# Optimization experiments

Measured on AMD Instinct MI355X. Metric: run time of the kernel, lower is better.

## Reference

```python
import jax, jax.numpy as jnp
import numpy as np

NUM_CLASSES = 19


def setup_inputs() -> dict:
    key = jax.random.key(0)
    k1, k2 = jax.random.split(key)
    B, H, W, G = 32, 1024, 1024, 32
    n_blocks = B * (H // G) * (W // G)  # 32768
    preds = jax.random.normal(k1, (n_blocks, NUM_CLASSES), dtype=jnp.float32)
    targets = jax.random.randint(k2, (B, H, W), 0, NUM_CLASSES, dtype=jnp.int32)
    return {"preds": preds, "targets": targets, "grid_size": G}


def _get_batch_label_vector(targets, num_classes, grid_size):
    # targets: [B,H,W] int labels. Pad with `num_classes` (a value outside the
    # histogram range [0, num_classes-1], matching torch.histc's exclusion).
    b, h, w = targets.shape
    pad_h = (-h) % grid_size
    pad_w = (-w) % grid_size
    t = jnp.pad(targets, ((0, 0), (0, pad_h), (0, pad_w)),
                constant_values=num_classes)
    H, W = h + pad_h, w + pad_w
    # -> [n_blocks, grid_size*grid_size] of per-cell labels
    t = t.reshape(b, H // grid_size, grid_size, W // grid_size, grid_size)
    t = t.transpose(0, 1, 3, 2, 4).reshape(-1, grid_size * grid_size)
    n = t.shape[0]
    # Multi-hot presence vector via scatter; padded value == num_classes is
    # out of range and dropped (mirrors histc ignoring out-of-range values).
    tvect = jnp.zeros((n, num_classes), jnp.float32)
    tvect = tvect.at[jnp.arange(n)[:, None], t].set(1.0, mode='drop')
    return tvect


def reference(preds, targets, grid_size):
    se_target = _get_batch_label_vector(targets, NUM_CLASSES, grid_size)
    # BCE(sigmoid(preds), se_target) with mean reduction, written stably:
    # log(sigmoid(x)) = log_sigmoid(x), log(1-sigmoid(x)) = log_sigmoid(-x)
    log_p = jax.nn.log_sigmoid(preds)
    log_1mp = jax.nn.log_sigmoid(-preds)
    loss = -(se_target * log_p + (1.0 - se_target) * log_1mp)
    return jnp.mean(loss)
```

## Files before the change

### kernel.cpp

```cpp
#include <hip/hip_runtime.h>

#define NUM_CLASSES 19
#define TILES_PER_WAVE 8
#define WAVES_PER_BLOCK 4

__global__ __launch_bounds__(256) void seg_loss_partial(
    const float* __restrict__ preds,
    const int*   __restrict__ targets,
    float*       __restrict__ partial)
{
    const int t    = threadIdx.x;
    const int wave = t >> 6;
    const int lane = t & 63;

    float loss = 0.0f;
    const int tile0 = (blockIdx.x * WAVES_PER_BLOCK + wave) * TILES_PER_WAVE;

    for (int i = 0; i < TILES_PER_WAVE; ++i) {
        const int n  = tile0 + i;
        const int b  = n >> 10;
        const int by = (n >> 5) & 31;
        const int bx = n & 31;
        const int* base = targets + ((long long)b << 20)
                                  + (long long)(by << 5) * 1024
                                  + (bx << 5);

        unsigned mask = 0u;
        #pragma unroll
        for (int j = 0; j < 4; ++j) {
            const int idx  = j * 64 + lane;
            const int row  = idx >> 3;
            const int quad = idx & 7;
            const int4 v = *(const int4*)(base + row * 1024 + quad * 4);
            mask |= (1u << v.x) | (1u << v.y) | (1u << v.z) | (1u << v.w);
        }

        mask |= __shfl_xor(mask, 1);
        mask |= __shfl_xor(mask, 2);
        mask |= __shfl_xor(mask, 4);
        mask |= __shfl_xor(mask, 8);
        mask |= __shfl_xor(mask, 16);
        mask |= __shfl_xor(mask, 32);

        if (lane < NUM_CLASSES) {
            const float x  = preds[n * NUM_CLASSES + lane];
            const float tv = ((mask >> lane) & 1u) ? 1.0f : 0.0f;
            const float sp = fmaxf(x, 0.0f) + log1pf(__expf(-fabsf(x)));
            loss += sp - tv * x;
        }
    }

    loss += __shfl_xor(loss, 1);
    loss += __shfl_xor(loss, 2);
    loss += __shfl_xor(loss, 4);
    loss += __shfl_xor(loss, 8);
    loss += __shfl_xor(loss, 16);
    loss += __shfl_xor(loss, 32);

    __shared__ float wsum[WAVES_PER_BLOCK];
    if (lane == 0) wsum[wave] = loss;
    __syncthreads();
    if (t == 0)
        partial[blockIdx.x] = wsum[0] + wsum[1] + wsum[2] + wsum[3];
}

__global__ __launch_bounds__(256) void seg_loss_reduce(
    const float* __restrict__ partial,
    float*       __restrict__ out,
    float inv_total, int n)
{
    float s = 0.0f;
    for (int i = threadIdx.x; i < n; i += 256) s += partial[i];

    s += __shfl_xor(s, 1);
    s += __shfl_xor(s, 2);
    s += __shfl_xor(s, 4);
    s += __shfl_xor(s, 8);
    s += __shfl_xor(s, 16);
    s += __shfl_xor(s, 32);

    __shared__ float wsum[4];
    const int wave = threadIdx.x >> 6;
    const int lane = threadIdx.x & 63;
    if (lane == 0) wsum[wave] = s;
    __syncthreads();
    if (threadIdx.x == 0)
        out[0] = (wsum[0] + wsum[1] + wsum[2] + wsum[3]) * inv_total;
}

extern "C" void kernel_launch(void* const* d_in, const int* in_sizes, int n_in,
                              void* d_out, int out_size, void* d_ws, size_t ws_size,
                              hipStream_t stream) {
    const float* preds   = (const float*)d_in[0];
    const int*   targets = (const int*)d_in[1];
    float*       out     = (float*)d_out;
    float*       partial = (float*)d_ws;

    const int n_tiles  = in_sizes[0] / NUM_CLASSES;
    const int n_blocks = n_tiles / (TILES_PER_WAVE * WAVES_PER_BLOCK);
    const float inv_total = 1.0f / (float)(n_tiles * NUM_CLASSES);

    seg_loss_partial<<<n_blocks, 256, 0, stream>>>(preds, targets, partial);
    seg_loss_reduce<<<1, 256, 0, stream>>>(partial, out, inv_total, n_blocks);
}
```

Measured before the change: 199.3 us.

## Map each block to a full 32-row image strip with contiguous row loads

Each block now covers one 32x1024 strip of the label image, which holds 32 grid tiles. On every iteration the 256 threads read one full contiguous 4 KB row, and 8 threads share each tile, so a tile's mask is merged with 3 shuffles and passed through shared memory. The loss is then spread across all 256 threads, with 8 threads per tile handling up to 3 classes each, instead of only 19 of 64 lanes. The aim is fully contiguous, wide memory accesses and better lane use during the loss math, at the cost of an extra shared-memory barrier.

```diff
diff --git a/kernel.cpp b/kernel.cpp
--- a/kernel.cpp
+++ b/kernel.cpp
@@ -1,50 +1,40 @@
 #include <hip/hip_runtime.h>
 
 #define NUM_CLASSES 19
-#define TILES_PER_WAVE 8
-#define WAVES_PER_BLOCK 4
 
 __global__ __launch_bounds__(256) void seg_loss_partial(
     const float* __restrict__ preds,
     const int*   __restrict__ targets,
     float*       __restrict__ partial)
 {
-    const int t    = threadIdx.x;
-    const int wave = t >> 6;
-    const int lane = t & 63;
+    const int tid = threadIdx.x;
+    const int* base = targets + (blockIdx.x << 15);
 
+    unsigned mask = 0u;
+    #pragma unroll 4
+    for (int r = 0; r < 32; ++r) {
+        const int4 v = *(const int4*)(base + (r << 10) + (tid << 2));
+        mask |= (1u << v.x) | (1u << v.y) | (1u << v.z) | (1u << v.w);
+    }
+
+    mask |= __shfl_xor(mask, 1);
+    mask |= __shfl_xor(mask, 2);
+    mask |= __shfl_xor(mask, 4);
+
+    __shared__ unsigned tile_mask[32];
+    if ((tid & 7) == 0) tile_mask[tid >> 3] = mask;
+    __syncthreads();
+
+    const int tile = tid >> 3;
+    const int n    = (blockIdx.x << 5) + tile;
+    const unsigned m = tile_mask[tile];
     float loss = 0.0f;
-    const int tile0 = (blockIdx.x * WAVES_PER_BLOCK + wave) * TILES_PER_WAVE;
-
-    for (int i = 0; i < TILES_PER_WAVE; ++i) {
-        const int n  = tile0 + i;
-        const int b  = n >> 10;
-        const int by = (n >> 5) & 31;
-        const int bx = n & 31;
-        const int* base = targets + ((long long)b << 20)
-                                  + (long long)(by << 5) * 1024
-                                  + (bx << 5);
-
-        unsigned mask = 0u;
-        #pragma unroll
-        for (int j = 0; j < 4; ++j) {
-            const int idx  = j * 64 + lane;
-            const int row  = idx >> 3;
-            const int quad = idx & 7;
-            const int4 v = *(const int4*)(base + row * 1024 + quad * 4);
-            mask |= (1u << v.x) | (1u << v.y) | (1u << v.z) | (1u << v.w);
-        }
-
-        mask |= __shfl_xor(mask, 1);
-        mask |= __shfl_xor(mask, 2);
-        mask |= __shfl_xor(mask, 4);
-        mask |= __shfl_xor(mask, 8);
-        mask |= __shfl_xor(mask, 16);
-        mask |= __shfl_xor(mask, 32);
-
-        if (lane < NUM_CLASSES) {
-            const float x  = preds[n * NUM_CLASSES + lane];
-            const float tv = ((mask >> lane) & 1u) ? 1.0f : 0.0f;
+    #pragma unroll
+    for (int j = 0; j < 3; ++j) {
+        const int c = (tid & 7) + (j << 3);
+        if (c < NUM_CLASSES) {
+            const float x  = preds[n * NUM_CLASSES + c];
+            const float tv = ((m >> c) & 1u) ? 1.0f : 0.0f;
             const float sp = fmaxf(x, 0.0f) + log1pf(__expf(-fabsf(x)));
             loss += sp - tv * x;
         }
@@ -57,20 +47,20 @@
     loss += __shfl_xor(loss, 16);
     loss += __shfl_xor(loss, 32);
 
-    __shared__ float wsum[WAVES_PER_BLOCK];
-    if (lane == 0) wsum[wave] = loss;
+    __shared__ float wsum[4];
+    if ((tid & 63) == 0) wsum[tid >> 6] = loss;
     __syncthreads();
-    if (t == 0)
+    if (tid == 0)
         partial[blockIdx.x] = wsum[0] + wsum[1] + wsum[2] + wsum[3];
 }
 
 __global__ __launch_bounds__(256) void seg_loss_reduce(
     const float* __restrict__ partial,
     float*       __restrict__ out,
-    float inv_total, int n)
+    float inv_total, int nblocks)
 {
     float s = 0.0f;
-    for (int i = threadIdx.x; i < n; i += 256) s += partial[i];
+    for (int i = threadIdx.x; i < nblocks; i += 256) s += partial[i];
 
     s += __shfl_xor(s, 1);
     s += __shfl_xor(s, 2);
@@ -97,7 +87,7 @@
     float*       partial = (float*)d_ws;
 
     const int n_tiles  = in_sizes[0] / NUM_CLASSES;
-    const int n_blocks = n_tiles / (TILES_PER_WAVE * WAVES_PER_BLOCK);
+    const int n_blocks = n_tiles / 32;
     const float inv_total = 1.0f / (float)(n_tiles * NUM_CLASSES);
 
     seg_loss_partial<<<n_blocks, 256, 0, stream>>>(preds, targets, partial);
```

Measured after the change: 197.7 us. No clear change (-0.8%).
